# Kernel optimization log

Hardware: AMD Instinct MI355X
Metric: run time of the kernel (lower is better)

Reference implementation:

```python
import jax, jax.numpy as jnp
import numpy as np

EPS = 1e-5  # torch BatchNorm1d default

def _bn(z, g, b):
    # training-mode BatchNorm1d: per-feature batch mean, biased variance
    m = jnp.mean(z, axis=0)
    v = jnp.mean((z - m) ** 2, axis=0)
    return (z - m) * jax.lax.rsqrt(v + EPS) * g + b

def _cell(x, h, c, Wx, Wh, gx, bx, gh, bh):
    gates = _bn(x @ Wx.T, gx, bx) + _bn(h @ Wh.T, gh, bh)  # [B, 4H]
    f, i, o, g = jnp.split(gates, 4, axis=1)  # chunk order f,i,o,g
    c2 = jax.nn.sigmoid(f) * c + jax.nn.sigmoid(i) * jnp.tanh(g)
    h2 = jax.nn.sigmoid(o) * jnp.tanh(c2)
    return h2, c2

def setup_inputs() -> dict:
    key = jax.random.key(0)
    B, H, OUT = 16384, 512, 256
    IN0 = 257  # input_size - 1 (x_dim 256 + y_dim 1)
    ks = jax.random.split(key, 16)
    def lin(k, fo, fi):
        s = 1.0 / np.sqrt(fi)
        return jax.random.uniform(k, (fo, fi), jnp.float32, -s, s)
    return {
        "x": jax.random.normal(ks[0], (B, 256), jnp.float32),
        "y": jax.random.normal(ks[1], (B, 1), jnp.float32),
        "h0": jax.random.normal(ks[2], (2, B, H), jnp.float32),
        "c0": jax.random.normal(ks[3], (2, B, H), jnp.float32),
        "Wx0": lin(ks[4], 4 * H, IN0),
        "Wh0": lin(ks[5], 4 * H, H),
        "gx0": jnp.ones((4 * H,), jnp.float32),
        "bx0": jnp.zeros((4 * H,), jnp.float32),
        "gh0": jnp.ones((4 * H,), jnp.float32),
        "bh0": jnp.zeros((4 * H,), jnp.float32),
        "Wx1": lin(ks[6], 4 * H, H),
        "Wh1": lin(ks[7], 4 * H, H),
        "gx1": jnp.ones((4 * H,), jnp.float32),
        "bx1": jnp.zeros((4 * H,), jnp.float32),
        "gh1": jnp.ones((4 * H,), jnp.float32),
        "bh1": jnp.zeros((4 * H,), jnp.float32),
        "Wo": lin(ks[8], OUT, H),
        "bo": jnp.zeros((OUT,), jnp.float32),
    }

def reference(x, y, h0, c0, Wx0, Wh0, gx0, bx0, gh0, bh0,
              Wx1, Wh1, gx1, bx1, gh1, bh1, Wo, bo):
    inp = jnp.concatenate([x, y], axis=1)  # [B, 257]
    h1, c1 = _cell(inp, h0[0], c0[0], Wx0, Wh0, gx0, bx0, gh0, bh0)
    h2, c2 = _cell(h1, h0[1], c0[1], Wx1, Wh1, gx1, bx1, gh1, bh1)
    out = h2 @ Wo.T + bo  # [B, output_size]
    return (out, jnp.stack([h1, h2]), jnp.stack([c1, c2]))
```

## Files before the change

### kernel.cpp

```cpp
#include <hip/hip_runtime.h>
#include <cstdint>

typedef unsigned short u16;
typedef unsigned int u32;
typedef float floatx4 __attribute__((ext_vector_type(4)));
typedef __bf16 bf16x8 __attribute__((ext_vector_type(8)));
typedef u16 u16x4 __attribute__((ext_vector_type(4)));

__device__ __forceinline__ u16 f2b(float f) {
  u32 u = __builtin_bit_cast(u32, f);
  u32 r = (u + 0x7fffu + ((u >> 16) & 1u)) >> 16;
  return (u16)r;
}
__device__ __forceinline__ float b2f(u16 b) {
  return __builtin_bit_cast(float, (u32)b << 16);
}
__device__ __forceinline__ u32 pkbf(float lo, float hi) {
  u32 r;
  asm("v_cvt_pk_bf16_f32 %0, %1, %2" : "=v"(r) : "v"(lo), "v"(hi));
  return r;
}
__device__ __forceinline__ float sigf(float x) { return 1.f / (1.f + __expf(-x)); }
__device__ __forceinline__ float tanhfast(float x) { return 2.f / (1.f + __expf(-2.f * x)) - 1.f; }

#define GLDS(gp, lp) __builtin_amdgcn_global_load_lds( \
    (const __attribute__((address_space(1))) u32*)(gp), \
    (__attribute__((address_space(3))) u32*)(lp), 16, 0, 0)

template <int KT>
__device__ __forceinline__ void gemm_body(
    const u16* __restrict__ A, const u16* __restrict__ W, u32* __restrict__ C32,
    int N, float* __restrict__ ssum, float* __restrict__ ssq, u16* lds) {
  constexpr int NT = KT / 32;
  const int tid = threadIdx.x;
  const int lane = tid & 63;
  const int wid = tid >> 6;
  const int wm = (wid >> 1) << 6;
  const int wn = (wid & 1) << 6;
  const int fr = lane & 15;
  const int fq = lane >> 4;

  const int l = blockIdx.x + (blockIdx.y << 4);
  const int xcd = l & 7;
  const int idx = l >> 3;
  const int bx = idx & 15;
  const int by = (xcd << 4) + (idx >> 4);
  const int m0 = by << 7;
  const int n0 = bx << 7;

  const u16* Ab = A + (size_t)m0 * KT;
  const u16* Wb = W + (size_t)n0 * KT;

  const int ra = tid >> 2;
  const int ca = (tid & 3) ^ ((ra >> 1) & 3);
  const u16* pa0 = Ab + (size_t)ra * KT + ca * 8;
  const u16* pa1 = pa0 + (size_t)64 * KT;
  const u16* pb0 = Wb + (size_t)ra * KT + ca * 8;
  const u16* pb1 = pb0 + (size_t)64 * KT;
  const int da = tid * 8;
  const int db = 4096 + tid * 8;

#define STAGE(kt) do {                                   \
    const int _sl = ((kt) % 3) * 8192;                   \
    const int _ko = (kt) * 32;                           \
    GLDS(pa0 + _ko, &lds[_sl + da]);                     \
    GLDS(pa1 + _ko, &lds[_sl + da + 2048]);              \
    GLDS(pb0 + _ko, &lds[_sl + db]);                     \
    GLDS(pb1 + _ko, &lds[_sl + db + 2048]);              \
  } while (0)

  int aoffs[4], boffs[4];
#pragma unroll
  for (int mf = 0; mf < 4; ++mf) {
    const int R = wm + mf * 16 + fr;
    aoffs[mf] = R * 32 + ((fq ^ ((R >> 1) & 3)) << 3);
  }
#pragma unroll
  for (int nf = 0; nf < 4; ++nf) {
    const int R = wn + nf * 16 + fr;
    boffs[nf] = 4096 + R * 32 + ((fq ^ ((R >> 1) & 3)) << 3);
  }

  floatx4 acc[4][4] = {};

  STAGE(0);
  STAGE(1);

#pragma unroll
  for (int t = 0; t < NT; ++t) {
    if (t == NT - 1) asm volatile("s_waitcnt vmcnt(0)" ::: "memory");
    else             asm volatile("s_waitcnt vmcnt(4)" ::: "memory");
    __builtin_amdgcn_s_barrier();
    __builtin_amdgcn_sched_barrier(0);

    if (t + 2 < NT) STAGE(t + 2);

    const int sl = (t % 3) * 8192;
    bf16x8 bfv[4];
#pragma unroll
    for (int nf = 0; nf < 4; ++nf) bfv[nf] = *(const bf16x8*)&lds[sl + boffs[nf]];
    __builtin_amdgcn_s_setprio(1);
#pragma unroll
    for (int mf = 0; mf < 4; ++mf) {
      const bf16x8 af = *(const bf16x8*)&lds[sl + aoffs[mf]];
#pragma unroll
      for (int nf = 0; nf < 4; ++nf)
        acc[mf][nf] = __builtin_amdgcn_mfma_f32_16x16x32_bf16(af, bfv[nf], acc[mf][nf], 0, 0, 0);
    }
    __builtin_amdgcn_s_setprio(0);
    asm volatile("s_waitcnt lgkmcnt(0)" ::: "memory");
    __builtin_amdgcn_sched_barrier(0);
  }
#undef STAGE

#pragma unroll
  for (int mf = 0; mf < 4; ++mf) {
    const int rp = (m0 + wm + mf * 16 + fq * 4) >> 1;
#pragma unroll
    for (int nf = 0; nf < 4; ++nf) {
      const int col = n0 + wn + nf * 16 + fr;
#pragma unroll
      for (int p = 0; p < 2; ++p)
        C32[(size_t)(rp + p) * N + col] = pkbf(acc[mf][nf][2 * p], acc[mf][nf][2 * p + 1]);
    }
  }
#pragma unroll
  for (int nf = 0; nf < 4; ++nf) {
    float s = 0.f, qv = 0.f;
#pragma unroll
    for (int mf = 0; mf < 4; ++mf)
#pragma unroll
      for (int r = 0; r < 4; ++r) {
        const float v = acc[mf][nf][r];
        s += v;
        qv += v * v;
      }
    s += __shfl_xor(s, 16);
    s += __shfl_xor(s, 32);
    qv += __shfl_xor(qv, 16);
    qv += __shfl_xor(qv, 32);
    if (fq == 0) {
      atomicAdd(&ssum[n0 + wn + nf * 16 + fr], s);
      atomicAdd(&ssq[n0 + wn + nf * 16 + fr], qv);
    }
  }
}

template <int KTX, int KTH>
__global__ __launch_bounds__(256) void gemm_pair(
    const u16* __restrict__ Ax, const u16* __restrict__ Wx, u32* __restrict__ Cx,
    float* __restrict__ ssx, float* __restrict__ sqx,
    const u16* __restrict__ Ah, const u16* __restrict__ Wh, u32* __restrict__ Ch,
    float* __restrict__ ssh, float* __restrict__ sqh, int N) {
  __shared__ __align__(16) u16 lds[3 * 8192];
  if (blockIdx.z == 0) gemm_body<KTX>(Ax, Wx, Cx, N, ssx, sqx, lds);
  else                 gemm_body<KTH>(Ah, Wh, Ch, N, ssh, sqh, lds);
}

__global__ __launch_bounds__(256) void gemm_out(
    const u16* __restrict__ A, const u16* __restrict__ W, float* __restrict__ C,
    int N, int K, const float* __restrict__ bias) {
  __shared__ u16 As[128 * 32];
  __shared__ u16 Bs[128 * 32];
  const int tid = threadIdx.x;
  const int lane = tid & 63;
  const int wave = tid >> 6;
  const int wm = (wave >> 1) << 6;
  const int wn = (wave & 1) << 6;
  const int m0 = blockIdx.y * 128;
  const int n0 = blockIdx.x * 128;
  const u16* Ab = A + (size_t)m0 * K;
  const u16* Wb = W + (size_t)n0 * K;
  const size_t soff = (size_t)(tid >> 2) * K + ((tid & 3) << 3);
  const size_t soff2 = soff + (size_t)64 * K;
  const int fr = lane & 15;
  const int fq = lane >> 4;
  const int aoff = fr * 32 + fq * 8;

  floatx4 acc[4][4] = {};

  for (int k0 = 0; k0 < K; k0 += 32) {
    __syncthreads();
    GLDS(Ab + soff + k0, &As[tid * 8]);
    GLDS(Ab + soff2 + k0, &As[tid * 8 + 2048]);
    GLDS(Wb + soff + k0, &Bs[tid * 8]);
    GLDS(Wb + soff2 + k0, &Bs[tid * 8 + 2048]);
    __syncthreads();
    bf16x8 af[4], bfv[4];
#pragma unroll
    for (int i = 0; i < 4; ++i) af[i] = *(const bf16x8*)&As[(wm + i * 16) * 32 + aoff];
#pragma unroll
    for (int j = 0; j < 4; ++j) bfv[j] = *(const bf16x8*)&Bs[(wn + j * 16) * 32 + aoff];
#pragma unroll
    for (int i = 0; i < 4; ++i)
#pragma unroll
      for (int j = 0; j < 4; ++j)
        acc[i][j] = __builtin_amdgcn_mfma_f32_16x16x32_bf16(af[i], bfv[j], acc[i][j], 0, 0, 0);
  }

#pragma unroll
  for (int i = 0; i < 4; ++i)
#pragma unroll
    for (int j = 0; j < 4; ++j) {
      const int col = n0 + wn + j * 16 + fr;
      const float bv = bias[col];
#pragma unroll
      for (int r = 0; r < 4; ++r) {
        const int row = m0 + wm + i * 16 + fq * 4 + r;
        C[(size_t)row * N + col] = acc[i][j][r] + bv;
      }
    }
}

__global__ void prep_inputs_k(const float* __restrict__ x, const float* __restrict__ y,
                              u16* __restrict__ inpb,
                              const float4* __restrict__ h0, u16x4* __restrict__ h0b) {
  const int bid = blockIdx.x;
  if (bid < 4608) {
    const int idx = bid * 256 + threadIdx.x;
    const int b = idx / 72;
    const int c4 = idx - b * 72;
    float4 v = make_float4(0.f, 0.f, 0.f, 0.f);
    if (c4 < 64) v = ((const float4*)x)[b * 64 + c4];
    else if (c4 == 64) v.x = y[b];
    u16x4 r;
    r.x = f2b(v.x); r.y = f2b(v.y); r.z = f2b(v.z); r.w = f2b(v.w);
    *(u16x4*)&inpb[b * 288 + c4 * 4] = r;
  } else {
    const int idx = (bid - 4608) * 256 + threadIdx.x;
    const float4 v = h0[idx];
    u16x4 r;
    r.x = f2b(v.x); r.y = f2b(v.y); r.z = f2b(v.z); r.w = f2b(v.w);
    h0b[idx] = r;
  }
}

__global__ void prep_weights_k(
    const float* __restrict__ Wx0, u16* __restrict__ wx0b,
    const float4* __restrict__ Wh0, u16x4* __restrict__ wh0b,
    const float4* __restrict__ Wx1, u16x4* __restrict__ wx1b,
    const float4* __restrict__ Wh1, u16x4* __restrict__ wh1b,
    const float4* __restrict__ Wo, u16x4* __restrict__ wob) {
  const int bid = blockIdx.x;
  if (bid < 2304) {
    const int idx = bid * 256 + threadIdx.x;
    const int r = idx / 288;
    const int c = idx - r * 288;
    wx0b[idx] = f2b(c < 257 ? Wx0[r * 257 + c] : 0.f);
    return;
  }
  const float4* src;
  u16x4* dst;
  int idx;
  if (bid < 2304 + 3072) {
    const int seg = (bid - 2304) >> 10;
    idx = ((bid - 2304) & 1023) * 256 + threadIdx.x;
    src = seg == 0 ? Wh0 : (seg == 1 ? Wx1 : Wh1);
    dst = seg == 0 ? wh0b : (seg == 1 ? wx1b : wh1b);
  } else {
    idx = (bid - 2304 - 3072) * 256 + threadIdx.x;
    src = Wo;
    dst = wob;
  }
  const float4 v = src[idx];
  u16x4 r;
  r.x = f2b(v.x); r.y = f2b(v.y); r.z = f2b(v.z); r.w = f2b(v.w);
  dst[idx] = r;
}

__global__ void coef_k(const float* __restrict__ st, const float* __restrict__ gx,
                       const float* __restrict__ bx, const float* __restrict__ gh,
                       const float* __restrict__ bh, float* __restrict__ cf, float invB) {
  const int j = blockIdx.x * 256 + threadIdx.x;
  const float mx = st[j] * invB;
  const float vx = st[2048 + j] * invB - mx * mx;
  const float ax = gx[j] * rsqrtf(vx + 1e-5f);
  const float mh = st[4096 + j] * invB;
  const float vh = st[6144 + j] * invB - mh * mh;
  const float ah = gh[j] * rsqrtf(vh + 1e-5f);
  cf[j] = ax;
  cf[2048 + j] = ah;
  cf[4096 + j] = bx[j] - mx * ax + bh[j] - mh * ah;
}

__global__ __launch_bounds__(256) void cell2_k(
    const u32* __restrict__ Zx, const u32* __restrict__ Zh,
    const float* __restrict__ coef, const float* __restrict__ cin,
    float* __restrict__ hout, float* __restrict__ cout, u16* __restrict__ hb) {
  const int idx = blockIdx.x * 256 + threadIdx.x;
  const int bp = idx >> 8;
  const int j2 = (idx & 255) << 1;
  const size_t zb = (size_t)bp << 11;
  float gv[4][2][2];
#pragma unroll
  for (int g = 0; g < 4; ++g) {
    const int col = (g << 9) + j2;
    const uint2 zx2 = *(const uint2*)&Zx[zb + col];
    const uint2 zh2 = *(const uint2*)&Zh[zb + col];
    const float2 ax = *(const float2*)&coef[col];
    const float2 ah = *(const float2*)&coef[2048 + col];
    const float2 cb = *(const float2*)&coef[4096 + col];
    gv[g][0][0] = ax.x * b2f((u16)zx2.x) + ah.x * b2f((u16)zh2.x) + cb.x;
    gv[g][1][0] = ax.x * b2f((u16)(zx2.x >> 16)) + ah.x * b2f((u16)(zh2.x >> 16)) + cb.x;
    gv[g][0][1] = ax.y * b2f((u16)zx2.y) + ah.y * b2f((u16)zh2.y) + cb.y;
    gv[g][1][1] = ax.y * b2f((u16)(zx2.y >> 16)) + ah.y * b2f((u16)(zh2.y >> 16)) + cb.y;
  }
#pragma unroll
  for (int s = 0; s < 2; ++s) {
    const int b = (bp << 1) + s;
    const size_t ob = ((size_t)b << 9) + j2;
    const float2 cp = *(const float2*)(cin + ob);
    float cn[2], hn[2];
#pragma unroll
    for (int t = 0; t < 2; ++t) {
      const float cprev = t ? cp.y : cp.x;
      const float cc = sigf(gv[0][s][t]) * cprev + sigf(gv[1][s][t]) * tanhfast(gv[3][s][t]);
      cn[t] = cc;
      hn[t] = sigf(gv[2][s][t]) * tanhfast(cc);
    }
    *(float2*)(cout + ob) = make_float2(cn[0], cn[1]);
    *(float2*)(hout + ob) = make_float2(hn[0], hn[1]);
    *(u32*)(hb + ob) = pkbf(hn[0], hn[1]);
  }
}

extern "C" void kernel_launch(void* const* d_in, const int* in_sizes, int n_in,
                              void* d_out, int out_size, void* d_ws, size_t ws_size,
                              hipStream_t stream) {
  (void)in_sizes; (void)n_in; (void)out_size; (void)ws_size;
  constexpr int B = 16384, H = 512, G = 2048, KP = 288, K1 = 512, NOUT = 256;

  const float* x = (const float*)d_in[0];
  const float* y = (const float*)d_in[1];
  const float* h0 = (const float*)d_in[2];
  const float* c0 = (const float*)d_in[3];
  const float* Wx0 = (const float*)d_in[4];
  const float* Wh0 = (const float*)d_in[5];
  const float* gx0 = (const float*)d_in[6];
  const float* bx0 = (const float*)d_in[7];
  const float* gh0 = (const float*)d_in[8];
  const float* bh0 = (const float*)d_in[9];
  const float* Wx1 = (const float*)d_in[10];
  const float* Wh1 = (const float*)d_in[11];
  const float* gx1 = (const float*)d_in[12];
  const float* bx1 = (const float*)d_in[13];
  const float* gh1 = (const float*)d_in[14];
  const float* bh1 = (const float*)d_in[15];
  const float* Wo = (const float*)d_in[16];
  const float* bo = (const float*)d_in[17];

  char* p = (char*)d_ws;
  u16* Zx = (u16*)p;   p += (size_t)B * G * 2;
  u16* Zh = (u16*)p;   p += (size_t)B * G * 2;
  u16* h0b = (u16*)p;  p += (size_t)2 * B * H * 2;
  u16* h1b = (u16*)p;  p += (size_t)B * H * 2;
  u16* inpb = (u16*)p; p += (size_t)B * KP * 2;
  u16* wx0b = (u16*)p; p += (size_t)G * KP * 2;
  u16* wh0b = (u16*)p; p += (size_t)G * K1 * 2;
  u16* wx1b = (u16*)p; p += (size_t)G * K1 * 2;
  u16* wh1b = (u16*)p; p += (size_t)G * K1 * 2;
  u16* wob = (u16*)p;  p += (size_t)NOUT * K1 * 2;
  float* stats = (float*)p; p += (size_t)8 * G * 4;
  float* coef = (float*)p;  p += (size_t)6 * G * 4;

  float* out_o = (float*)d_out;
  float* h_o = out_o + (size_t)B * NOUT;
  float* c_o = h_o + (size_t)2 * B * H;

  hipMemsetAsync(stats, 0, (size_t)8 * G * sizeof(float), stream);

  prep_inputs_k<<<4608 + 16384, 256, 0, stream>>>(x, y, inpb, (const float4*)h0, (u16x4*)h0b);
  prep_weights_k<<<2304 + 3072 + 128, 256, 0, stream>>>(
      Wx0, wx0b, (const float4*)Wh0, (u16x4*)wh0b, (const float4*)Wx1, (u16x4*)wx1b,
      (const float4*)Wh1, (u16x4*)wh1b, (const float4*)Wo, (u16x4*)wob);

  const dim3 blk(256);
  const dim3 gpair(G / 128, B / 128, 2);

  gemm_pair<KP, K1><<<gpair, blk, 0, stream>>>(
      inpb, wx0b, (u32*)Zx, stats + 0 * G, stats + 1 * G,
      h0b, wh0b, (u32*)Zh, stats + 2 * G, stats + 3 * G, G);
  coef_k<<<G / 256, 256, 0, stream>>>(stats, gx0, bx0, gh0, bh0, coef, 1.f / B);
  cell2_k<<<B / 2, 256, 0, stream>>>((const u32*)Zx, (const u32*)Zh, coef, c0, h_o, c_o, h1b);

  gemm_pair<K1, K1><<<gpair, blk, 0, stream>>>(
      h1b, wx1b, (u32*)Zx, stats + 4 * G, stats + 5 * G,
      h0b + (size_t)B * H, wh1b, (u32*)Zh, stats + 6 * G, stats + 7 * G, G);
  coef_k<<<G / 256, 256, 0, stream>>>(stats + 4 * G, gx1, bx1, gh1, bh1, coef + 3 * G, 1.f / B);
  cell2_k<<<B / 2, 256, 0, stream>>>((const u32*)Zx, (const u32*)Zh, coef + 3 * G,
                                     c0 + (size_t)B * H, h_o + (size_t)B * H,
                                     c_o + (size_t)B * H, h1b);

  const dim3 gout(NOUT / 128, B / 128);
  gemm_out<<<gout, blk, 0, stream>>>(h1b, wob, out_o, NOUT, K1, bo);
}
```

Measured before the change: 540.5 us.

## Widen gate GEMM tiles to 128x256 with 8 waves and per-XCD BN stat slices

The paired gate GEMM moves from 128x128 tiles with 4 waves to 128x256 tiles with 512 threads (8 waves). Each A tile is now reused across twice as many output columns, which cuts global and LDS traffic per FLOP. The LDS ring slots grow to fit the wider B tile, and the load count per stage and the vmcnt waits are adjusted to match. BatchNorm sum and sum-of-squares atomics now go to 8 per-XCD copies that coef_k adds together, which spreads out atomic contention at the cost of a larger memset and extra reads. The larger block and LDS footprint may reduce occupancy.

```diff
diff --git a/kernel.cpp b/kernel.cpp
--- a/kernel.cpp
+++ b/kernel.cpp
@@ -32,21 +32,22 @@
     const u16* __restrict__ A, const u16* __restrict__ W, u32* __restrict__ C32,
     int N, float* __restrict__ ssum, float* __restrict__ ssq, u16* lds) {
   constexpr int NT = KT / 32;
+  constexpr int SLOT = 12288;
   const int tid = threadIdx.x;
   const int lane = tid & 63;
   const int wid = tid >> 6;
-  const int wm = (wid >> 1) << 6;
-  const int wn = (wid & 1) << 6;
+  const int wm = (wid >> 2) << 6;
+  const int wn = (wid & 3) << 6;
   const int fr = lane & 15;
   const int fq = lane >> 4;
 
-  const int l = blockIdx.x + (blockIdx.y << 4);
+  const int l = blockIdx.x + (blockIdx.y << 3);
   const int xcd = l & 7;
   const int idx = l >> 3;
-  const int bx = idx & 15;
-  const int by = (xcd << 4) + (idx >> 4);
+  const int bx = idx & 7;
+  const int by = (xcd << 4) + (idx >> 3);
   const int m0 = by << 7;
-  const int n0 = bx << 7;
+  const int n0 = bx << 8;
 
   const u16* Ab = A + (size_t)m0 * KT;
   const u16* Wb = W + (size_t)n0 * KT;
@@ -54,19 +55,17 @@
   const int ra = tid >> 2;
   const int ca = (tid & 3) ^ ((ra >> 1) & 3);
   const u16* pa0 = Ab + (size_t)ra * KT + ca * 8;
-  const u16* pa1 = pa0 + (size_t)64 * KT;
   const u16* pb0 = Wb + (size_t)ra * KT + ca * 8;
-  const u16* pb1 = pb0 + (size_t)64 * KT;
+  const u16* pb1 = pb0 + (size_t)128 * KT;
   const int da = tid * 8;
   const int db = 4096 + tid * 8;
 
 #define STAGE(kt) do {                                   \
-    const int _sl = ((kt) % 3) * 8192;                   \
+    const int _sl = ((kt) % 3) * SLOT;                   \
     const int _ko = (kt) * 32;                           \
     GLDS(pa0 + _ko, &lds[_sl + da]);                     \
-    GLDS(pa1 + _ko, &lds[_sl + da + 2048]);              \
     GLDS(pb0 + _ko, &lds[_sl + db]);                     \
-    GLDS(pb1 + _ko, &lds[_sl + db + 2048]);              \
+    GLDS(pb1 + _ko, &lds[_sl + db + 4096]);              \
   } while (0)
 
   int aoffs[4], boffs[4];
@@ -89,13 +88,13 @@
 #pragma unroll
   for (int t = 0; t < NT; ++t) {
     if (t == NT - 1) asm volatile("s_waitcnt vmcnt(0)" ::: "memory");
-    else             asm volatile("s_waitcnt vmcnt(4)" ::: "memory");
+    else             asm volatile("s_waitcnt vmcnt(3)" ::: "memory");
     __builtin_amdgcn_s_barrier();
     __builtin_amdgcn_sched_barrier(0);
 
     if (t + 2 < NT) STAGE(t + 2);
 
-    const int sl = (t % 3) * 8192;
+    const int sl = (t % 3) * SLOT;
     bf16x8 bfv[4];
 #pragma unroll
     for (int nf = 0; nf < 4; ++nf) bfv[nf] = *(const bf16x8*)&lds[sl + boffs[nf]];
@@ -124,6 +123,8 @@
         C32[(size_t)(rp + p) * N + col] = pkbf(acc[mf][nf][2 * p], acc[mf][nf][2 * p + 1]);
     }
   }
+  float* ss = ssum + xcd * 2048;
+  float* sq = ssq + xcd * 2048;
 #pragma unroll
   for (int nf = 0; nf < 4; ++nf) {
     float s = 0.f, qv = 0.f;
@@ -140,19 +141,19 @@
     qv += __shfl_xor(qv, 16);
     qv += __shfl_xor(qv, 32);
     if (fq == 0) {
-      atomicAdd(&ssum[n0 + wn + nf * 16 + fr], s);
-      atomicAdd(&ssq[n0 + wn + nf * 16 + fr], qv);
+      atomicAdd(&ss[n0 + wn + nf * 16 + fr], s);
+      atomicAdd(&sq[n0 + wn + nf * 16 + fr], qv);
     }
   }
 }
 
 template <int KTX, int KTH>
-__global__ __launch_bounds__(256) void gemm_pair(
+__global__ __launch_bounds__(512, 4) void gemm_pair(
     const u16* __restrict__ Ax, const u16* __restrict__ Wx, u32* __restrict__ Cx,
     float* __restrict__ ssx, float* __restrict__ sqx,
     const u16* __restrict__ Ah, const u16* __restrict__ Wh, u32* __restrict__ Ch,
     float* __restrict__ ssh, float* __restrict__ sqh, int N) {
-  __shared__ __align__(16) u16 lds[3 * 8192];
+  __shared__ __align__(16) u16 lds[3 * 12288];
   if (blockIdx.z == 0) gemm_body<KTX>(Ax, Wx, Cx, N, ssx, sqx, lds);
   else                 gemm_body<KTH>(Ah, Wh, Ch, N, ssh, sqh, lds);
 }
@@ -271,12 +272,21 @@
 __global__ void coef_k(const float* __restrict__ st, const float* __restrict__ gx,
                        const float* __restrict__ bx, const float* __restrict__ gh,
                        const float* __restrict__ bh, float* __restrict__ cf, float invB) {
+  constexpr int SH = 8 * 2048;
   const int j = blockIdx.x * 256 + threadIdx.x;
-  const float mx = st[j] * invB;
-  const float vx = st[2048 + j] * invB - mx * mx;
+  float sx = 0.f, qx = 0.f, sh = 0.f, qh = 0.f;
+#pragma unroll
+  for (int s = 0; s < 8; ++s) {
+    sx += st[0 * SH + s * 2048 + j];
+    qx += st[1 * SH + s * 2048 + j];
+    sh += st[2 * SH + s * 2048 + j];
+    qh += st[3 * SH + s * 2048 + j];
+  }
+  const float mx = sx * invB;
+  const float vx = qx * invB - mx * mx;
   const float ax = gx[j] * rsqrtf(vx + 1e-5f);
-  const float mh = st[4096 + j] * invB;
-  const float vh = st[6144 + j] * invB - mh * mh;
+  const float mh = sh * invB;
+  const float vh = qh * invB - mh * mh;
   const float ah = gh[j] * rsqrtf(vh + 1e-5f);
   cf[j] = ax;
   cf[2048 + j] = ah;
@@ -329,6 +339,7 @@
                               hipStream_t stream) {
   (void)in_sizes; (void)n_in; (void)out_size; (void)ws_size;
   constexpr int B = 16384, H = 512, G = 2048, KP = 288, K1 = 512, NOUT = 256;
+  constexpr int SH = 8 * 2048;
 
   const float* x = (const float*)d_in[0];
   const float* y = (const float*)d_in[1];
@@ -360,37 +371,38 @@
   u16* wx1b = (u16*)p; p += (size_t)G * K1 * 2;
   u16* wh1b = (u16*)p; p += (size_t)G * K1 * 2;
   u16* wob = (u16*)p;  p += (size_t)NOUT * K1 * 2;
-  float* stats = (float*)p; p += (size_t)8 * G * 4;
+  float* stats = (float*)p; p += (size_t)8 * SH * 4;
   float* coef = (float*)p;  p += (size_t)6 * G * 4;
 
   float* out_o = (float*)d_out;
   float* h_o = out_o + (size_t)B * NOUT;
   float* c_o = h_o + (size_t)2 * B * H;
 
-  hipMemsetAsync(stats, 0, (size_t)8 * G * sizeof(float), stream);
+  hipMemsetAsync(stats, 0, (size_t)8 * SH * sizeof(float), stream);
 
   prep_inputs_k<<<4608 + 16384, 256, 0, stream>>>(x, y, inpb, (const float4*)h0, (u16x4*)h0b);
   prep_weights_k<<<2304 + 3072 + 128, 256, 0, stream>>>(
       Wx0, wx0b, (const float4*)Wh0, (u16x4*)wh0b, (const float4*)Wx1, (u16x4*)wx1b,
       (const float4*)Wh1, (u16x4*)wh1b, (const float4*)Wo, (u16x4*)wob);
 
-  const dim3 blk(256);
-  const dim3 gpair(G / 128, B / 128, 2);
-
-  gemm_pair<KP, K1><<<gpair, blk, 0, stream>>>(
-      inpb, wx0b, (u32*)Zx, stats + 0 * G, stats + 1 * G,
-      h0b, wh0b, (u32*)Zh, stats + 2 * G, stats + 3 * G, G);
+  const dim3 blk512(512);
+  const dim3 gpair(G / 256, B / 128, 2);
+
+  gemm_pair<KP, K1><<<gpair, blk512, 0, stream>>>(
+      inpb, wx0b, (u32*)Zx, stats + 0 * SH, stats + 1 * SH,
+      h0b, wh0b, (u32*)Zh, stats + 2 * SH, stats + 3 * SH, G);
   coef_k<<<G / 256, 256, 0, stream>>>(stats, gx0, bx0, gh0, bh0, coef, 1.f / B);
   cell2_k<<<B / 2, 256, 0, stream>>>((const u32*)Zx, (const u32*)Zh, coef, c0, h_o, c_o, h1b);
 
-  gemm_pair<K1, K1><<<gpair, blk, 0, stream>>>(
-      h1b, wx1b, (u32*)Zx, stats + 4 * G, stats + 5 * G,
-      h0b + (size_t)B * H, wh1b, (u32*)Zh, stats + 6 * G, stats + 7 * G, G);
-  coef_k<<<G / 256, 256, 0, stream>>>(stats + 4 * G, gx1, bx1, gh1, bh1, coef + 3 * G, 1.f / B);
+  gemm_pair<K1, K1><<<gpair, blk512, 0, stream>>>(
+      h1b, wx1b, (u32*)Zx, stats + 4 * SH, stats + 5 * SH,
+      h0b + (size_t)B * H, wh1b, (u32*)Zh, stats + 6 * SH, stats + 7 * SH, G);
+  coef_k<<<G / 256, 256, 0, stream>>>(stats + 4 * SH, gx1, bx1, gh1, bh1, coef + 3 * G, 1.f / B);
   cell2_k<<<B / 2, 256, 0, stream>>>((const u32*)Zx, (const u32*)Zh, coef + 3 * G,
                                      c0 + (size_t)B * H, h_o + (size_t)B * H,
                                      c_o + (size_t)B * H, h1b);
 
+  const dim3 blk(256);
   const dim3 gout(NOUT / 128, B / 128);
   gemm_out<<<gout, blk, 0, stream>>>(h1b, wob, out_o, NOUT, K1, bo);
 }
```

Result: faster. 528.0 us (-2.3%).
